# Kernel tuning notes

Measured on AMD Instinct MI355X. Metric: run time of the kernel, lower is better.

## Reference

```python
import jax, jax.numpy as jnp
import numpy as np

B = 16384          # graphs per batch
NUM_NODES = 32     # nodes per graph
EMBED = 64         # embed_dim (GCNConv in=out, conv1mult=1)
DEG = 8            # avg in-graph degree
OUT = 2            # outputSize
N = B * NUM_NODES
E = N * DEG
HID = NUM_NODES * EMBED  # size_in1 = size_out1 = 2048


def setup_inputs() -> dict:
    key = jax.random.key(0)
    ks = jax.random.split(key, 10)
    x = jax.random.normal(ks[0], (N, EMBED), dtype=jnp.float32)
    # edges constrained within each graph of NUM_NODES nodes
    offs = jnp.repeat(jnp.arange(B, dtype=jnp.int64) * NUM_NODES, DEG * NUM_NODES)
    src = jax.random.randint(ks[1], (E,), 0, NUM_NODES, dtype=jnp.int64) + offs
    dst = jax.random.randint(ks[2], (E,), 0, NUM_NODES, dtype=jnp.int64) + offs
    edge_index = jnp.stack([src, dst], axis=0)
    batch = jnp.repeat(jnp.arange(B, dtype=jnp.int64), NUM_NODES)
    s = 0.05
    Wc = jax.random.normal(ks[3], (EMBED, EMBED), dtype=jnp.float32) * s
    bc = jnp.zeros((EMBED,), dtype=jnp.float32)
    W1 = jax.random.normal(ks[4], (HID, HID), dtype=jnp.float32) * (1.0 / np.sqrt(HID))
    b1 = jnp.zeros((HID,), dtype=jnp.float32)
    W2 = jax.random.normal(ks[5], (OUT, HID), dtype=jnp.float32) * (1.0 / np.sqrt(HID))
    b2 = jnp.zeros((OUT,), dtype=jnp.float32)
    return {"x": x, "Wc": Wc, "bc": bc, "W1": W1, "b1": b1,
            "W2": W2, "b2": b2, "edge_index": edge_index, "batch": batch}


def gcn_conv(x, Wc, bc, edge_index):
    # PyG GCNConv: linear transform, add self-loops, symmetric normalization,
    # scatter-add aggregation at target nodes, then bias.
    n = x.shape[0]
    h = x @ Wc.T                                        # [N, F]
    loop = jnp.arange(n, dtype=edge_index.dtype)
    row = jnp.concatenate([edge_index[0], loop])        # sources
    col = jnp.concatenate([edge_index[1], loop])        # targets
    deg = jax.ops.segment_sum(jnp.ones_like(col, dtype=h.dtype), col,
                              num_segments=n)           # in-degree incl. self-loop
    dinv = jnp.where(deg > 0, jax.lax.rsqrt(deg), 0.0)
    norm = dinv[row] * dinv[col]                        # [E+N]
    msgs = h[row] * norm[:, None]                       # gather + scale
    out = jax.ops.segment_sum(msgs, col, num_segments=n)  # scatter-add
    return out + bc


def reference(x, Wc, bc, W1, b1, W2, b2, edge_index, batch):
    h = gcn_conv(x, Wc, bc, edge_index)
    h = jax.nn.relu(h)
    h = h.reshape(B, HID)                # [B, numNodes*embed_dim]
    h = h @ W1.T + b1                    # lin1 (dropout is eval-mode identity)
    h = jax.nn.relu(h)
    h = h @ W2.T + b2                    # lin2
    return jax.nn.softmax(h, axis=-1)    # [B, OUT]
```

## Files before the change

kernel.cpp:

```cpp
#include <hip/hip_runtime.h>

#define NGRAPH 16384
#define NNODE  32
#define EMB    64
#define HIDDIM 2048
#define ETOT   4194304
#define EPG    256

typedef __attribute__((ext_vector_type(8))) short bf16x8_t;
typedef __attribute__((ext_vector_type(8))) unsigned short u16x8_t;
typedef __attribute__((ext_vector_type(4))) float f32x4_t;

__device__ __forceinline__ unsigned short f2bf(float v) {
  unsigned int u = __float_as_uint(v);
  u += 0x7fffu + ((u >> 16) & 1u);
  return (unsigned short)(u >> 16);
}
__device__ __forceinline__ float bf2f(unsigned short u) {
  return __uint_as_float(((unsigned int)u) << 16);
}
__device__ __forceinline__ unsigned int cvtpk(float lo, float hi) {
  unsigned int r;
  asm("v_cvt_pk_bf16_f32 %0, %1, %2" : "=v"(r) : "v"(lo), "v"(hi));
  return r;
}
__device__ __forceinline__ bf16x8_t pack8(float4 a, float4 b) {
  union { unsigned int u[4]; bf16x8_t v; } r;
  r.u[0] = cvtpk(a.x, a.y); r.u[1] = cvtpk(a.z, a.w);
  r.u[2] = cvtpk(b.x, b.y); r.u[3] = cvtpk(b.z, b.w);
  return r.v;
}

#define GLDS(SRC, DST)                                                          \
  __builtin_amdgcn_global_load_lds(                                             \
      (const __attribute__((address_space(1))) void*)(SRC),                     \
      (__attribute__((address_space(3))) void*)(DST), 16, 0, 0)

__global__ __launch_bounds__(256) void cvt_w1(const float* __restrict__ W,
                                              unsigned short* __restrict__ Wb) {
  __shared__ float row[HIDDIM];
  const int r = blockIdx.x, t = threadIdx.x;
  const float4* p = (const float4*)(W + (size_t)r * HIDDIM);
  *(float4*)&row[t * 8]     = p[t * 2];
  *(float4*)&row[t * 8 + 4] = p[t * 2 + 1];
  __syncthreads();
  const int feat = t >> 2, nb = (t & 3) * 8;
  u16x8_t o;
  #pragma unroll
  for (int j = 0; j < 8; ++j) o[j] = f2bf(row[(nb + j) * 64 + feat]);
  *(u16x8_t*)(Wb + (size_t)r * HIDDIM + t * 8) = o;
}

__global__ __launch_bounds__(256, 4) void gcn_kernel(const float* __restrict__ x,
                                                     const float* __restrict__ Wc,
                                                     const float* __restrict__ bc,
                                                     const int* __restrict__ ei,
                                                     unsigned short* __restrict__ abf) {
  __shared__ __align__(16) char smem[40960];
  const int wv = threadIdx.x >> 6, lane = threadIdx.x & 63;
  const int g = blockIdx.x * 4 + wv;
  char* my = smem + wv * 10240;
  unsigned int*   adjcnt = (unsigned int*)my;
  unsigned short* adjb   = (unsigned short*)my;
  unsigned short* outT   = (unsigned short*)my;
  unsigned short* hT     = (unsigned short*)(my + 5120);
  const int lr = lane & 15, lk = lane >> 4;

  const float* xg = x + (size_t)g * (NNODE * EMB);
  float4 xr[2][2][2];
  #pragma unroll
  for (int mt = 0; mt < 2; ++mt)
    #pragma unroll
    for (int kk = 0; kk < 2; ++kk) {
      const float* p = xg + (mt * 16 + lr) * EMB + kk * 32 + lk * 8;
      xr[mt][kk][0] = *(const float4*)p;
      xr[mt][kk][1] = *(const float4*)(p + 4);
    }

  int sl[4], dl[4];
  #pragma unroll
  for (int j = 0; j < 4; ++j) {
    sl[j] = ei[(size_t)g * EPG + j * 64 + lane] - g * NNODE;
    dl[j] = ei[(size_t)ETOT + (size_t)g * EPG + j * 64 + lane] - g * NNODE;
  }

  {
    uint4 z = {0u, 0u, 0u, 0u};
    #pragma unroll
    for (int i = 0; i < 4; ++i) *(uint4*)&adjcnt[lane * 16 + i * 4] = z;
  }
  asm volatile("" ::: "memory");
  #pragma unroll
  for (int j = 0; j < 4; ++j) atomicAdd(&adjcnt[dl[j] * 32 + sl[j]], 1u);
  asm volatile("" ::: "memory");

  const int rr = lane >> 1, hh = lane & 1;
  uint4 c[4];
  unsigned int cs = 0;
  #pragma unroll
  for (int i = 0; i < 4; ++i) {
    c[i] = *(const uint4*)&adjcnt[rr * 32 + hh * 16 + i * 4];
    cs += c[i].x + c[i].y + c[i].z + c[i].w;
  }
  cs += (unsigned int)__shfl_xor((int)cs, 1);
  const float dinvr = rsqrtf(1.0f + (float)cs);
  asm volatile("" ::: "memory");
  {
    float vals[16];
    #pragma unroll
    for (int i = 0; i < 4; ++i) {
      const unsigned int cc[4] = {c[i].x, c[i].y, c[i].z, c[i].w};
      #pragma unroll
      for (int e = 0; e < 4; ++e) {
        const int s = hh * 16 + i * 4 + e;
        const float ds = __shfl(dinvr, s * 2);
        const float cnt = (float)cc[e] + ((s == rr) ? 1.0f : 0.0f);
        vals[i * 4 + e] = cnt * dinvr * ds;
      }
    }
    union { unsigned int u[8]; u16x8_t v[2]; } pk;
    #pragma unroll
    for (int i = 0; i < 8; ++i) pk.u[i] = cvtpk(vals[2 * i], vals[2 * i + 1]);
    *(u16x8_t*)&adjb[rr * 40 + hh * 16]     = pk.v[0];
    *(u16x8_t*)&adjb[rr * 40 + hh * 16 + 8] = pk.v[1];
  }

  bf16x8_t xa[2][2];
  #pragma unroll
  for (int mt = 0; mt < 2; ++mt)
    #pragma unroll
    for (int kk = 0; kk < 2; ++kk) xa[mt][kk] = pack8(xr[mt][kk][0], xr[mt][kk][1]);
  f32x4_t hc[2][4];
  #pragma unroll
  for (int mt = 0; mt < 2; ++mt)
    #pragma unroll
    for (int nt = 0; nt < 4; ++nt) hc[mt][nt] = (f32x4_t){0.f, 0.f, 0.f, 0.f};
  #pragma unroll
  for (int nt = 0; nt < 4; ++nt)
    #pragma unroll
    for (int kk = 0; kk < 2; ++kk) {
      const float* p = Wc + (nt * 16 + lr) * EMB + kk * 32 + lk * 8;
      const bf16x8_t wb = pack8(*(const float4*)p, *(const float4*)(p + 4));
      #pragma unroll
      for (int mt = 0; mt < 2; ++mt)
        hc[mt][nt] = __builtin_amdgcn_mfma_f32_16x16x32_bf16(xa[mt][kk], wb, hc[mt][nt], 0, 0, 0);
    }
  #pragma unroll
  for (int mt = 0; mt < 2; ++mt)
    #pragma unroll
    for (int nt = 0; nt < 4; ++nt) {
      uint2 pk;
      pk.x = cvtpk(hc[mt][nt][0], hc[mt][nt][1]);
      pk.y = cvtpk(hc[mt][nt][2], hc[mt][nt][3]);
      *(uint2*)&hT[(nt * 16 + lr) * 40 + mt * 16 + lk * 4] = pk;
    }
  asm volatile("" ::: "memory");

  bf16x8_t aj[2];
  #pragma unroll
  for (int mt = 0; mt < 2; ++mt)
    aj[mt] = *(const bf16x8_t*)&adjb[(mt * 16 + lr) * 40 + lk * 8];
  f32x4_t oc[2][4];
  #pragma unroll
  for (int mt = 0; mt < 2; ++mt)
    #pragma unroll
    for (int nt = 0; nt < 4; ++nt) oc[mt][nt] = (f32x4_t){0.f, 0.f, 0.f, 0.f};
  #pragma unroll
  for (int nt = 0; nt < 4; ++nt) {
    const bf16x8_t hb = *(const bf16x8_t*)&hT[(nt * 16 + lr) * 40 + lk * 8];
    #pragma unroll
    for (int mt = 0; mt < 2; ++mt)
      oc[mt][nt] = __builtin_amdgcn_mfma_f32_16x16x32_bf16(aj[mt], hb, oc[mt][nt], 0, 0, 0);
  }
  asm volatile("" ::: "memory");

  #pragma unroll
  for (int nt = 0; nt < 4; ++nt) {
    const float bcv = bc[nt * 16 + lr];
    #pragma unroll
    for (int mt = 0; mt < 2; ++mt) {
      float v0 = fmaxf(oc[mt][nt][0] + bcv, 0.0f);
      float v1 = fmaxf(oc[mt][nt][1] + bcv, 0.0f);
      float v2 = fmaxf(oc[mt][nt][2] + bcv, 0.0f);
      float v3 = fmaxf(oc[mt][nt][3] + bcv, 0.0f);
      uint2 pk;
      pk.x = cvtpk(v0, v1);
      pk.y = cvtpk(v2, v3);
      *(uint2*)&outT[(nt * 16 + lr) * 40 + mt * 16 + lk * 4] = pk;
    }
  }
  asm volatile("" ::: "memory");

  unsigned short* og = abf + (size_t)g * HIDDIM;
  #pragma unroll
  for (int j = 0; j < 4; ++j) {
    const int e = lane * 8 + j * 512;
    const int feat = e >> 5, nb = e & 31;
    *(u16x8_t*)(og + e) = *(const u16x8_t*)&outT[feat * 40 + nb];
  }
}

__global__ __launch_bounds__(512, 1) void lin1_kernel(const unsigned short* __restrict__ A,
                                                      const unsigned short* __restrict__ Bw,
                                                      const float* __restrict__ b1,
                                                      unsigned short* __restrict__ C) {
  __shared__ __align__(16) unsigned short sh[65536];

  const int bid = blockIdx.x;
  const int xcd = bid & 7;
  const int g = bid >> 3;
  const int bm = xcd * 8 + (g >> 3);
  const int bn = g & 7;

  const int tid = threadIdx.x;
  const int lane = tid & 63, w = tid >> 6;
  const int wm = w >> 2, wn = w & 3;
  const int lr = lane & 15, lk = lane >> 4;

  const int r0 = tid >> 3;
  const int kge = ((((tid & 7) * 16) ^ ((r0 & 7) << 4)) >> 1);
  const unsigned short* gA = A  + (size_t)(bm * 256 + r0) * HIDDIM + kge;
  const unsigned short* gB = Bw + (size_t)(bn * 256 + r0) * HIDDIM + kge;

  auto stage = [&](const unsigned short* gb, int d, int mat, int half, int tile) {
    const unsigned short* s = gb + (size_t)(half * 128) * HIDDIM + tile * 64;
    unsigned short* l = &sh[d * 32768 + mat * 16384 + half * 8192 + tid * 8];
    GLDS(s, l);
    GLDS(s + (size_t)64 * HIDDIM, l + 4096);
  };

  const int arow = wm * 8192 + lr * 64;
  const int brow = 16384 + (wn >> 1) * 8192 + ((wn & 1) * 64 + lr) * 64;
  int eoff[2];
  eoff[0] = (lk * 8) ^ ((lr & 7) << 3);
  eoff[1] = (32 + lk * 8) ^ ((lr & 7) << 3);

  f32x4_t acc[8][4];
  #pragma unroll
  for (int i = 0; i < 8; ++i)
    #pragma unroll
    for (int j = 0; j < 4; ++j) acc[i][j] = (f32x4_t){0.f, 0.f, 0.f, 0.f};

  stage(gA, 0, 0, 0, 0); stage(gA, 0, 0, 1, 0);
  stage(gB, 0, 1, 0, 0); stage(gB, 0, 1, 1, 0);
  stage(gB, 1, 1, 0, 1); stage(gB, 1, 1, 1, 1);
  asm volatile("s_waitcnt vmcnt(4)" ::: "memory");
  __builtin_amdgcn_sched_barrier(0);
  __builtin_amdgcn_s_barrier();

  bf16x8_t af[4][2], bv0[2][2], bv1[2][2];

  for (int it = 0; it < 16; ++it) {
    const int o = 2 * it + 1;
    const bool more = (it < 15);

    #pragma unroll
    for (int half = 0; half < 2; ++half) {
      const int dof = half * 32768;

      #pragma unroll
      for (int mi = 0; mi < 4; ++mi) {
        af[mi][0] = *(const bf16x8_t*)&sh[dof + arow + mi * 1024 + eoff[0]];
        af[mi][1] = *(const bf16x8_t*)&sh[dof + arow + mi * 1024 + eoff[1]];
      }
      #pragma unroll
      for (int ni = 0; ni < 2; ++ni) {
        bv0[ni][0] = *(const bf16x8_t*)&sh[dof + brow + ni * 1024 + eoff[0]];
        bv0[ni][1] = *(const bf16x8_t*)&sh[dof + brow + ni * 1024 + eoff[1]];
      }
      if (half == 0) stage(gA, 1, 0, 0, o);
      else if (more) stage(gA, 0, 0, 0, o + 1);
      asm volatile("s_waitcnt lgkmcnt(0)" ::: "memory");
      __builtin_amdgcn_sched_barrier(0);
      __builtin_amdgcn_s_barrier();
      __builtin_amdgcn_s_setprio(1);
      #pragma unroll
      for (int kk = 0; kk < 2; ++kk)
        #pragma unroll
        for (int mi = 0; mi < 4; ++mi)
          #pragma unroll
          for (int ni = 0; ni < 2; ++ni)
            acc[mi][ni] = __builtin_amdgcn_mfma_f32_16x16x32_bf16(af[mi][kk], bv0[ni][kk], acc[mi][ni], 0, 0, 0);
      __builtin_amdgcn_s_setprio(0);

      #pragma unroll
      for (int ni = 0; ni < 2; ++ni) {
        bv1[ni][0] = *(const bf16x8_t*)&sh[dof + brow + (ni + 2) * 1024 + eoff[0]];
        bv1[ni][1] = *(const bf16x8_t*)&sh[dof + brow + (ni + 2) * 1024 + eoff[1]];
      }
      if (half == 0) stage(gA, 1, 0, 1, o);
      else if (more) stage(gA, 0, 0, 1, o + 1);
      asm volatile("s_waitcnt lgkmcnt(0)" ::: "memory");
      __builtin_amdgcn_sched_barrier(0);
      __builtin_amdgcn_s_barrier();
      __builtin_amdgcn_s_setprio(1);
      #pragma unroll
      for (int kk = 0; kk < 2; ++kk)
        #pragma unroll
        for (int mi = 0; mi < 4; ++mi)
          #pragma unroll
          for (int ni = 0; ni < 2; ++ni)
            acc[mi][ni + 2] = __builtin_amdgcn_mfma_f32_16x16x32_bf16(af[mi][kk], bv1[ni][kk], acc[mi][ni + 2], 0, 0, 0);
      __builtin_amdgcn_s_setprio(0);

      #pragma unroll
      for (int mi = 0; mi < 4; ++mi) {
        af[mi][0] = *(const bf16x8_t*)&sh[dof + arow + (mi + 4) * 1024 + eoff[0]];
        af[mi][1] = *(const bf16x8_t*)&sh[dof + arow + (mi + 4) * 1024 + eoff[1]];
      }
      if (more) stage(gB, half, 1, 0, (half == 0) ? (o + 1) : (o + 2));
      asm volatile("s_waitcnt lgkmcnt(0)" ::: "memory");
      __builtin_amdgcn_sched_barrier(0);
      __builtin_amdgcn_s_barrier();
      __builtin_amdgcn_s_setprio(1);
      #pragma unroll
      for (int kk = 0; kk < 2; ++kk)
        #pragma unroll
        for (int mi = 0; mi < 4; ++mi)
          #pragma unroll
          for (int ni = 0; ni < 2; ++ni)
            acc[mi + 4][ni + 2] = __builtin_amdgcn_mfma_f32_16x16x32_bf16(af[mi][kk], bv1[ni][kk], acc[mi + 4][ni + 2], 0, 0, 0);
      __builtin_amdgcn_s_setprio(0);

      if (more) stage(gB, half, 1, 1, (half == 0) ? (o + 1) : (o + 2));
      asm volatile("s_waitcnt lgkmcnt(0)" ::: "memory");
      if (more) { asm volatile("s_waitcnt vmcnt(4)" ::: "memory"); }
      else      { asm volatile("s_waitcnt vmcnt(0)" ::: "memory"); }
      __builtin_amdgcn_sched_barrier(0);
      __builtin_amdgcn_s_barrier();
      __builtin_amdgcn_s_setprio(1);
      #pragma unroll
      for (int kk = 0; kk < 2; ++kk)
        #pragma unroll
        for (int mi = 0; mi < 4; ++mi)
          #pragma unroll
          for (int ni = 0; ni < 2; ++ni)
            acc[mi + 4][ni] = __builtin_amdgcn_mfma_f32_16x16x32_bf16(af[mi][kk], bv0[ni][kk], acc[mi + 4][ni], 0, 0, 0);
      __builtin_amdgcn_s_setprio(0);
    }
  }

  const int crow0 = bm * 256 + wm * 128 + lk * 4;
  const int ccol0 = bn * 256 + wn * 64 + lr;
  float b1v[4];
  #pragma unroll
  for (int ni = 0; ni < 4; ++ni) b1v[ni] = b1[ccol0 + ni * 16];
  #pragma unroll
  for (int mi = 0; mi < 8; ++mi)
    #pragma unroll
    for (int r = 0; r < 4; ++r) {
      unsigned short* cp = C + (size_t)(crow0 + mi * 16 + r) * HIDDIM + ccol0;
      #pragma unroll
      for (int ni = 0; ni < 4; ++ni) {
        const float v = acc[mi][ni][r] + b1v[ni];
        cp[ni * 16] = f2bf(v > 0.0f ? v : 0.0f);
      }
    }
}

__global__ __launch_bounds__(256) void lin2_kernel(const unsigned short* __restrict__ h1,
                                                   const float* __restrict__ W2,
                                                   const float* __restrict__ b2,
                                                   float* __restrict__ out) {
  const int gid = blockIdx.x * 4 + (threadIdx.x >> 6);
  const int lane = threadIdx.x & 63;
  const u16x8_t* hp = (const u16x8_t*)(h1 + (size_t)gid * HIDDIM);
  const float4* w0 = (const float4*)W2;
  const float4* w1 = (const float4*)(W2 + HIDDIM);
  float s0 = 0.0f, s1 = 0.0f;
  #pragma unroll
  for (int i = 0; i < 4; ++i) {
    const int idx = i * 64 + lane;
    const u16x8_t hv = hp[idx];
    const float4 a0 = w0[2 * idx], a1 = w0[2 * idx + 1];
    const float4 b0 = w1[2 * idx], b1 = w1[2 * idx + 1];
    const float f0 = bf2f(hv[0]), f1 = bf2f(hv[1]), f2 = bf2f(hv[2]), f3 = bf2f(hv[3]);
    const float f4 = bf2f(hv[4]), f5 = bf2f(hv[5]), f6 = bf2f(hv[6]), f7 = bf2f(hv[7]);
    s0 += f0 * a0.x + f1 * a0.y + f2 * a0.z + f3 * a0.w
        + f4 * a1.x + f5 * a1.y + f6 * a1.z + f7 * a1.w;
    s1 += f0 * b0.x + f1 * b0.y + f2 * b0.z + f3 * b0.w
        + f4 * b1.x + f5 * b1.y + f6 * b1.z + f7 * b1.w;
  }
  #pragma unroll
  for (int off = 32; off > 0; off >>= 1) {
    s0 += __shfl_down(s0, off);
    s1 += __shfl_down(s1, off);
  }
  if (lane == 0) {
    const float l0 = s0 + b2[0];
    const float l1 = s1 + b2[1];
    const float mx = fmaxf(l0, l1);
    const float e0 = expf(l0 - mx);
    const float e1 = expf(l1 - mx);
    const float inv = 1.0f / (e0 + e1);
    out[(size_t)gid * 2]     = e0 * inv;
    out[(size_t)gid * 2 + 1] = e1 * inv;
  }
}

extern "C" void kernel_launch(void* const* d_in, const int* in_sizes, int n_in,
                              void* d_out, int out_size, void* d_ws, size_t ws_size,
                              hipStream_t stream) {
  const float* x  = (const float*)d_in[0];
  const float* Wc = (const float*)d_in[1];
  const float* bc = (const float*)d_in[2];
  const float* W1 = (const float*)d_in[3];
  const float* b1 = (const float*)d_in[4];
  const float* W2 = (const float*)d_in[5];
  const float* b2 = (const float*)d_in[6];
  const int* ei   = (const int*)d_in[7];

  unsigned short* Abf  = (unsigned short*)d_ws;
  unsigned short* W1bf = (unsigned short*)((char*)d_ws + (size_t)67108864);
  unsigned short* h1   = (unsigned short*)((char*)d_ws + (size_t)75497472);

  cvt_w1<<<dim3(2048), dim3(256), 0, stream>>>(W1, W1bf);
  gcn_kernel<<<dim3(NGRAPH / 4), dim3(256), 0, stream>>>(x, Wc, bc, ei, Abf);
  lin1_kernel<<<dim3(512), dim3(512), 0, stream>>>(Abf, W1bf, b1, h1);
  lin2_kernel<<<dim3(4096), dim3(256), 0, stream>>>(h1, W2, b2, (float*)d_out);
}
```

Measured before the change: 185.0 us.

## Switch lin1 GEMM to 32x32x16 MFMA with fragment-ordered LDS staging

```diff
diff --git a/kernel.cpp b/kernel.cpp
--- a/kernel.cpp
+++ b/kernel.cpp
@@ -10,6 +10,7 @@
 typedef __attribute__((ext_vector_type(8))) short bf16x8_t;
 typedef __attribute__((ext_vector_type(8))) unsigned short u16x8_t;
 typedef __attribute__((ext_vector_type(4))) float f32x4_t;
+typedef __attribute__((ext_vector_type(16))) float f32x16_t;
 
 __device__ __forceinline__ unsigned short f2bf(float v) {
   unsigned int u = __float_as_uint(v);
@@ -215,12 +216,15 @@
   const int tid = threadIdx.x;
   const int lane = tid & 63, w = tid >> 6;
   const int wm = w >> 2, wn = w & 3;
-  const int lr = lane & 15, lk = lane >> 4;
-
-  const int r0 = tid >> 3;
-  const int kge = ((((tid & 7) * 16) ^ ((r0 & 7) << 4)) >> 1);
-  const unsigned short* gA = A  + (size_t)(bm * 256 + r0) * HIDDIM + kge;
-  const unsigned short* gB = Bw + (size_t)(bn * 256 + r0) * HIDDIM + kge;
+  const int l31 = lane & 31, lhi = lane >> 5;
+
+  const int sl_l  = tid & 63;
+  const int sl_mt = tid >> 8;
+  const int sl_ks = (tid >> 6) & 3;
+  const int srow = sl_mt * 32 + (sl_l & 31);
+  const int skel = sl_ks * 16 + (sl_l >> 5) * 8;
+  const unsigned short* gA = A  + (size_t)(bm * 256 + srow) * HIDDIM + skel;
+  const unsigned short* gB = Bw + (size_t)(bn * 256 + srow) * HIDDIM + skel;
 
   auto stage = [&](const unsigned short* gb, int d, int mat, int half, int tile) {
     const unsigned short* s = gb + (size_t)(half * 128) * HIDDIM + tile * 64;
@@ -229,17 +233,16 @@
     GLDS(s + (size_t)64 * HIDDIM, l + 4096);
   };
 
-  const int arow = wm * 8192 + lr * 64;
-  const int brow = 16384 + (wn >> 1) * 8192 + ((wn & 1) * 64 + lr) * 64;
-  int eoff[2];
-  eoff[0] = (lk * 8) ^ ((lr & 7) << 3);
-  eoff[1] = (32 + lk * 8) ^ ((lr & 7) << 3);
-
-  f32x4_t acc[8][4];
-  #pragma unroll
-  for (int i = 0; i < 8; ++i)
-    #pragma unroll
-    for (int j = 0; j < 4; ++j) acc[i][j] = (f32x4_t){0.f, 0.f, 0.f, 0.f};
+  const int abase = wm * 8192 + lane * 8;
+  const int bbase = 16384 + (wn >> 1) * 8192 + (wn & 1) * 4096 + lane * 8;
+
+  f32x16_t acc[4][2];
+  #pragma unroll
+  for (int i = 0; i < 4; ++i)
+    #pragma unroll
+    for (int j = 0; j < 2; ++j)
+      #pragma unroll
+      for (int r = 0; r < 16; ++r) acc[i][j][r] = 0.f;
 
   stage(gA, 0, 0, 0, 0); stage(gA, 0, 0, 1, 0);
   stage(gB, 0, 1, 0, 0); stage(gB, 0, 1, 1, 0);
@@ -248,7 +251,7 @@
   __builtin_amdgcn_sched_barrier(0);
   __builtin_amdgcn_s_barrier();
 
-  bf16x8_t af[4][2], bv0[2][2], bv1[2][2];
+  bf16x8_t af[4], bv[2][4];
 
   for (int it = 0; it < 16; ++it) {
     const int o = 2 * it + 1;
@@ -259,15 +262,13 @@
       const int dof = half * 32768;
 
       #pragma unroll
-      for (int mi = 0; mi < 4; ++mi) {
-        af[mi][0] = *(const bf16x8_t*)&sh[dof + arow + mi * 1024 + eoff[0]];
-        af[mi][1] = *(const bf16x8_t*)&sh[dof + arow + mi * 1024 + eoff[1]];
-      }
-      #pragma unroll
-      for (int ni = 0; ni < 2; ++ni) {
-        bv0[ni][0] = *(const bf16x8_t*)&sh[dof + brow + ni * 1024 + eoff[0]];
-        bv0[ni][1] = *(const bf16x8_t*)&sh[dof + brow + ni * 1024 + eoff[1]];
-      }
+      for (int ks = 0; ks < 4; ++ks)
+        af[ks] = *(const bf16x8_t*)&sh[dof + abase + ks * 512];
+      #pragma unroll
+      for (int nt = 0; nt < 2; ++nt)
+        #pragma unroll
+        for (int ks = 0; ks < 4; ++ks)
+          bv[nt][ks] = *(const bf16x8_t*)&sh[dof + bbase + nt * 2048 + ks * 512];
       if (half == 0) stage(gA, 1, 0, 0, o);
       else if (more) stage(gA, 0, 0, 0, o + 1);
       asm volatile("s_waitcnt lgkmcnt(0)" ::: "memory");
@@ -275,85 +276,57 @@
       __builtin_amdgcn_s_barrier();
       __builtin_amdgcn_s_setprio(1);
       #pragma unroll
-      for (int kk = 0; kk < 2; ++kk)
+      for (int ks = 0; ks < 4; ++ks)
         #pragma unroll
-        for (int mi = 0; mi < 4; ++mi)
+        for (int nt = 0; nt < 2; ++nt)
+          acc[0][nt] = __builtin_amdgcn_mfma_f32_32x32x16_bf16(af[ks], bv[nt][ks], acc[0][nt], 0, 0, 0);
+      __builtin_amdgcn_s_setprio(0);
+
+      #pragma unroll
+      for (int mt = 1; mt < 4; ++mt) {
+        #pragma unroll
+        for (int ks = 0; ks < 4; ++ks)
+          af[ks] = *(const bf16x8_t*)&sh[dof + abase + (mt * 4 + ks) * 512];
+        if (mt == 1) {
+          if (half == 0) stage(gA, 1, 0, 1, o);
+          else if (more) stage(gA, 0, 0, 1, o + 1);
+        } else if (mt == 2) {
+          if (more) stage(gB, half, 1, 0, (half == 0) ? (o + 1) : (o + 2));
+        } else {
+          if (more) stage(gB, half, 1, 1, (half == 0) ? (o + 1) : (o + 2));
+        }
+        asm volatile("s_waitcnt lgkmcnt(0)" ::: "memory");
+        if (mt == 3) {
+          if (more) { asm volatile("s_waitcnt vmcnt(4)" ::: "memory"); }
+          else      { asm volatile("s_waitcnt vmcnt(0)" ::: "memory"); }
+        }
+        __builtin_amdgcn_sched_barrier(0);
+        __builtin_amdgcn_s_barrier();
+        __builtin_amdgcn_s_setprio(1);
+        #pragma unroll
+        for (int ks = 0; ks < 4; ++ks)
           #pragma unroll
-          for (int ni = 0; ni < 2; ++ni)
-            acc[mi][ni] = __builtin_amdgcn_mfma_f32_16x16x32_bf16(af[mi][kk], bv0[ni][kk], acc[mi][ni], 0, 0, 0);
-      __builtin_amdgcn_s_setprio(0);
-
-      #pragma unroll
-      for (int ni = 0; ni < 2; ++ni) {
-        bv1[ni][0] = *(const bf16x8_t*)&sh[dof + brow + (ni + 2) * 1024 + eoff[0]];
-        bv1[ni][1] = *(const bf16x8_t*)&sh[dof + brow + (ni + 2) * 1024 + eoff[1]];
+          for (int nt = 0; nt < 2; ++nt)
+            acc[mt][nt] = __builtin_amdgcn_mfma_f32_32x32x16_bf16(af[ks], bv[nt][ks], acc[mt][nt], 0, 0, 0);
+        __builtin_amdgcn_s_setprio(0);
       }
-      if (half == 0) stage(gA, 1, 0, 1, o);
-      else if (more) stage(gA, 0, 0, 1, o + 1);
-      asm volatile("s_waitcnt lgkmcnt(0)" ::: "memory");
-      __builtin_amdgcn_sched_barrier(0);
-      __builtin_amdgcn_s_barrier();
-      __builtin_amdgcn_s_setprio(1);
-      #pragma unroll
-      for (int kk = 0; kk < 2; ++kk)
-        #pragma unroll
-        for (int mi = 0; mi < 4; ++mi)
-          #pragma unroll
-          for (int ni = 0; ni < 2; ++ni)
-            acc[mi][ni + 2] = __builtin_amdgcn_mfma_f32_16x16x32_bf16(af[mi][kk], bv1[ni][kk], acc[mi][ni + 2], 0, 0, 0);
-      __builtin_amdgcn_s_setprio(0);
-
-      #pragma unroll
-      for (int mi = 0; mi < 4; ++mi) {
-        af[mi][0] = *(const bf16x8_t*)&sh[dof + arow + (mi + 4) * 1024 + eoff[0]];
-        af[mi][1] = *(const bf16x8_t*)&sh[dof + arow + (mi + 4) * 1024 + eoff[1]];
-      }
-      if (more) stage(gB, half, 1, 0, (half == 0) ? (o + 1) : (o + 2));
-      asm volatile("s_waitcnt lgkmcnt(0)" ::: "memory");
-      __builtin_amdgcn_sched_barrier(0);
-      __builtin_amdgcn_s_barrier();
-      __builtin_amdgcn_s_setprio(1);
-      #pragma unroll
-      for (int kk = 0; kk < 2; ++kk)
-        #pragma unroll
-        for (int mi = 0; mi < 4; ++mi)
-          #pragma unroll
-          for (int ni = 0; ni < 2; ++ni)
-            acc[mi + 4][ni + 2] = __builtin_amdgcn_mfma_f32_16x16x32_bf16(af[mi][kk], bv1[ni][kk], acc[mi + 4][ni + 2], 0, 0, 0);
-      __builtin_amdgcn_s_setprio(0);
-
-      if (more) stage(gB, half, 1, 1, (half == 0) ? (o + 1) : (o + 2));
-      asm volatile("s_waitcnt lgkmcnt(0)" ::: "memory");
-      if (more) { asm volatile("s_waitcnt vmcnt(4)" ::: "memory"); }
-      else      { asm volatile("s_waitcnt vmcnt(0)" ::: "memory"); }
-      __builtin_amdgcn_sched_barrier(0);
-      __builtin_amdgcn_s_barrier();
-      __builtin_amdgcn_s_setprio(1);
-      #pragma unroll
-      for (int kk = 0; kk < 2; ++kk)
-        #pragma unroll
-        for (int mi = 0; mi < 4; ++mi)
-          #pragma unroll
-          for (int ni = 0; ni < 2; ++ni)
-            acc[mi + 4][ni] = __builtin_amdgcn_mfma_f32_16x16x32_bf16(af[mi][kk], bv0[ni][kk], acc[mi + 4][ni], 0, 0, 0);
-      __builtin_amdgcn_s_setprio(0);
-    }
-  }
-
-  const int crow0 = bm * 256 + wm * 128 + lk * 4;
-  const int ccol0 = bn * 256 + wn * 64 + lr;
-  float b1v[4];
-  #pragma unroll
-  for (int ni = 0; ni < 4; ++ni) b1v[ni] = b1[ccol0 + ni * 16];
-  #pragma unroll
-  for (int mi = 0; mi < 8; ++mi)
-    #pragma unroll
-    for (int r = 0; r < 4; ++r) {
-      unsigned short* cp = C + (size_t)(crow0 + mi * 16 + r) * HIDDIM + ccol0;
-      #pragma unroll
-      for (int ni = 0; ni < 4; ++ni) {
-        const float v = acc[mi][ni][r] + b1v[ni];
-        cp[ni * 16] = f2bf(v > 0.0f ? v : 0.0f);
+    }
+  }
+
+  const int crow0 = bm * 256 + wm * 128;
+  const int ccol0 = bn * 256 + wn * 64;
+  float b1v[2];
+  b1v[0] = b1[ccol0 + l31];
+  b1v[1] = b1[ccol0 + 32 + l31];
+  #pragma unroll
+  for (int mt = 0; mt < 4; ++mt)
+    #pragma unroll
+    for (int nt = 0; nt < 2; ++nt) {
+      #pragma unroll
+      for (int r = 0; r < 16; ++r) {
+        const int row = crow0 + mt * 32 + (r & 3) + 8 * (r >> 2) + 4 * lhi;
+        const float v = acc[mt][nt][r] + b1v[nt];
+        C[(size_t)row * HIDDIM + ccol0 + nt * 32 + l31] = f2bf(v > 0.0f ? v : 0.0f);
       }
     }
 }
```

New measurement: 211.6 us. 1.14x slower.

## Fuse lin2 projection into lin1 epilogue with atomic logit accumulation

Applied to the files above, without the earlier changes.

```diff
diff --git a/kernel.cpp b/kernel.cpp
--- a/kernel.cpp
+++ b/kernel.cpp
@@ -37,9 +37,11 @@
       (__attribute__((address_space(3))) void*)(DST), 16, 0, 0)
 
 __global__ __launch_bounds__(256) void cvt_w1(const float* __restrict__ W,
-                                              unsigned short* __restrict__ Wb) {
+                                              unsigned short* __restrict__ Wb,
+                                              float* __restrict__ logits) {
   __shared__ float row[HIDDIM];
   const int r = blockIdx.x, t = threadIdx.x;
+  if (r < 128) logits[r * 256 + t] = 0.0f;
   const float4* p = (const float4*)(W + (size_t)r * HIDDIM);
   *(float4*)&row[t * 8]     = p[t * 2];
   *(float4*)&row[t * 8 + 4] = p[t * 2 + 1];
@@ -203,7 +205,8 @@
 __global__ __launch_bounds__(512, 1) void lin1_kernel(const unsigned short* __restrict__ A,
                                                       const unsigned short* __restrict__ Bw,
                                                       const float* __restrict__ b1,
-                                                      unsigned short* __restrict__ C) {
+                                                      const float* __restrict__ W2,
+                                                      float* __restrict__ logits) {
   __shared__ __align__(16) unsigned short sh[65536];
 
   const int bid = blockIdx.x;
@@ -342,60 +345,52 @@
 
   const int crow0 = bm * 256 + wm * 128 + lk * 4;
   const int ccol0 = bn * 256 + wn * 64 + lr;
-  float b1v[4];
-  #pragma unroll
-  for (int ni = 0; ni < 4; ++ni) b1v[ni] = b1[ccol0 + ni * 16];
+  float b1v[4], w2a[4], w2b[4];
+  #pragma unroll
+  for (int ni = 0; ni < 4; ++ni) {
+    b1v[ni] = b1[ccol0 + ni * 16];
+    w2a[ni] = W2[ccol0 + ni * 16];
+    w2b[ni] = W2[HIDDIM + ccol0 + ni * 16];
+  }
   #pragma unroll
   for (int mi = 0; mi < 8; ++mi)
     #pragma unroll
     for (int r = 0; r < 4; ++r) {
-      unsigned short* cp = C + (size_t)(crow0 + mi * 16 + r) * HIDDIM + ccol0;
+      float s0 = 0.0f, s1 = 0.0f;
       #pragma unroll
       for (int ni = 0; ni < 4; ++ni) {
-        const float v = acc[mi][ni][r] + b1v[ni];
-        cp[ni * 16] = f2bf(v > 0.0f ? v : 0.0f);
-      }
-    }
-}
-
-__global__ __launch_bounds__(256) void lin2_kernel(const unsigned short* __restrict__ h1,
-                                                   const float* __restrict__ W2,
-                                                   const float* __restrict__ b2,
-                                                   float* __restrict__ out) {
-  const int gid = blockIdx.x * 4 + (threadIdx.x >> 6);
-  const int lane = threadIdx.x & 63;
-  const u16x8_t* hp = (const u16x8_t*)(h1 + (size_t)gid * HIDDIM);
-  const float4* w0 = (const float4*)W2;
-  const float4* w1 = (const float4*)(W2 + HIDDIM);
-  float s0 = 0.0f, s1 = 0.0f;
-  #pragma unroll
-  for (int i = 0; i < 4; ++i) {
-    const int idx = i * 64 + lane;
-    const u16x8_t hv = hp[idx];
-    const float4 a0 = w0[2 * idx], a1 = w0[2 * idx + 1];
-    const float4 b0 = w1[2 * idx], b1 = w1[2 * idx + 1];
-    const float f0 = bf2f(hv[0]), f1 = bf2f(hv[1]), f2 = bf2f(hv[2]), f3 = bf2f(hv[3]);
-    const float f4 = bf2f(hv[4]), f5 = bf2f(hv[5]), f6 = bf2f(hv[6]), f7 = bf2f(hv[7]);
-    s0 += f0 * a0.x + f1 * a0.y + f2 * a0.z + f3 * a0.w
-        + f4 * a1.x + f5 * a1.y + f6 * a1.z + f7 * a1.w;
-    s1 += f0 * b0.x + f1 * b0.y + f2 * b0.z + f3 * b0.w
-        + f4 * b1.x + f5 * b1.y + f6 * b1.z + f7 * b1.w;
-  }
-  #pragma unroll
-  for (int off = 32; off > 0; off >>= 1) {
-    s0 += __shfl_down(s0, off);
-    s1 += __shfl_down(s1, off);
-  }
-  if (lane == 0) {
-    const float l0 = s0 + b2[0];
-    const float l1 = s1 + b2[1];
-    const float mx = fmaxf(l0, l1);
-    const float e0 = expf(l0 - mx);
-    const float e1 = expf(l1 - mx);
-    const float inv = 1.0f / (e0 + e1);
-    out[(size_t)gid * 2]     = e0 * inv;
-    out[(size_t)gid * 2 + 1] = e1 * inv;
-  }
+        const float v = fmaxf(acc[mi][ni][r] + b1v[ni], 0.0f);
+        s0 = fmaf(v, w2a[ni], s0);
+        s1 = fmaf(v, w2b[ni], s1);
+      }
+      #pragma unroll
+      for (int off = 1; off < 16; off <<= 1) {
+        s0 += __shfl_xor(s0, off);
+        s1 += __shfl_xor(s1, off);
+      }
+      if (lr == 0) {
+        const int row = crow0 + mi * 16 + r;
+        atomicAdd(&logits[row * 2],     s0);
+        atomicAdd(&logits[row * 2 + 1], s1);
+      }
+    }
+}
+
+__global__ __launch_bounds__(256) void softmax_kernel(const float* __restrict__ logits,
+                                                      const float* __restrict__ b2,
+                                                      float* __restrict__ out) {
+  const int i = blockIdx.x * 256 + threadIdx.x;
+  const float2 lg = *((const float2*)logits + i);
+  const float l0 = lg.x + b2[0];
+  const float l1 = lg.y + b2[1];
+  const float mx = fmaxf(l0, l1);
+  const float e0 = expf(l0 - mx);
+  const float e1 = expf(l1 - mx);
+  const float inv = 1.0f / (e0 + e1);
+  float2 o;
+  o.x = e0 * inv;
+  o.y = e1 * inv;
+  *((float2*)out + i) = o;
 }
 
 extern "C" void kernel_launch(void* const* d_in, const int* in_sizes, int n_in,
@@ -410,12 +405,12 @@
   const float* b2 = (const float*)d_in[6];
   const int* ei   = (const int*)d_in[7];
 
-  unsigned short* Abf  = (unsigned short*)d_ws;
-  unsigned short* W1bf = (unsigned short*)((char*)d_ws + (size_t)67108864);
-  unsigned short* h1   = (unsigned short*)((char*)d_ws + (size_t)75497472);
-
-  cvt_w1<<<dim3(2048), dim3(256), 0, stream>>>(W1, W1bf);
+  unsigned short* Abf    = (unsigned short*)d_ws;
+  unsigned short* W1bf   = (unsigned short*)((char*)d_ws + (size_t)67108864);
+  float*          logits = (float*)((char*)d_ws + (size_t)75497472);
+
+  cvt_w1<<<dim3(2048), dim3(256), 0, stream>>>(W1, W1bf, logits);
   gcn_kernel<<<dim3(NGRAPH / 4), dim3(256), 0, stream>>>(x, Wc, bc, ei, Abf);
-  lin1_kernel<<<dim3(512), dim3(512), 0, stream>>>(Abf, W1bf, b1, h1);
-  lin2_kernel<<<dim3(4096), dim3(256), 0, stream>>>(h1, W2, b2, (float*)d_out);
-}
+  lin1_kernel<<<dim3(512), dim3(512), 0, stream>>>(Abf, W1bf, b1, W2, logits);
+  softmax_kernel<<<dim3(64), dim3(256), 0, stream>>>(logits, b2, (float*)d_out);
+}
```

Result: slower. 242.0 us (+30.8%).
